# Optimization experiments

Hardware: AMD Instinct MI355X
Metric: run time of the kernel (lower is better)

Reference implementation:

```python
import jax, jax.numpy as jnp
import numpy as np

N = 400000        # pixel nodes (B images ~224x224)
E = 3200000       # edges, avg degree 8
B = 8             # images
NUM_SP = 150      # superpixels per image (<= 196, per assert)
S = B * NUM_SP    # total superpixel segments
GRID = 14 * 14    # fixed 14x14 grid = 196 slots
DIMS = [24, 8, 16, 32, 64, 64]  # conv_out_dim=24 -> channels//8 ... channels=64


def setup_inputs():
    key = jax.random.key(0)
    ks = jax.random.split(key, 16)
    inp = {}
    inp["x"] = jax.random.normal(ks[0], (N, DIMS[0]), jnp.float32)
    inp["edge_index"] = jax.random.randint(ks[1], (2, E), 0, N, jnp.int32)
    inp["batch_idx"] = jnp.sort(jax.random.randint(ks[2], (N,), 0, S, jnp.int32))
    inp["num_sp"] = jnp.full((B,), NUM_SP, jnp.int32)
    for i in range(5):
        fi, fo = DIMS[i], DIMS[i + 1]
        inp[f"W{i+1}"] = jax.random.normal(ks[3 + i], (fi, fo), jnp.float32) * (2.0 / fi) ** 0.5
        inp[f"b{i+1}"] = jnp.zeros((fo,), jnp.float32)
        inp[f"g{i+1}"] = jnp.ones((fo,), jnp.float32)
        inp[f"be{i+1}"] = jnp.zeros((fo,), jnp.float32)
    C = DIMS[-1]
    inp["Wp"] = jax.random.normal(ks[9], (4 * C, C), jnp.float32) * (2.0 / (4 * C)) ** 0.5
    inp["bp"] = jnp.zeros((C,), jnp.float32)
    return inp


def _forward(x, edge_index, batch_idx, num_sp, layers, Wp, bp):
    n = x.shape[0]
    # GCNConv: add self-loops, symmetric normalization D^-1/2 (A+I) D^-1/2
    loop = jnp.arange(n, dtype=edge_index.dtype)
    src = jnp.concatenate([edge_index[0], loop])
    dst = jnp.concatenate([edge_index[1], loop])
    deg = jax.ops.segment_sum(jnp.ones_like(dst, dtype=jnp.float32), dst, num_segments=n)
    dis = jax.lax.rsqrt(deg)  # deg >= 1 due to self-loops
    norm = dis[src] * dis[dst]  # [E+N]

    h = x
    for i, (W, b, g, be) in enumerate(layers):
        h = h @ W                                                   # [N, fo]
        h = jax.ops.segment_sum(h[src] * norm[:, None], dst, num_segments=n) + b
        # BatchNorm (training mode: batch stats over all nodes)
        mu = h.mean(axis=0)
        var = h.var(axis=0)
        h = g * (h - mu) * jax.lax.rsqrt(var + 1e-5) + be
        if i < 4:  # last BN feeds the aggregator directly (no ReLU)
            h = jax.nn.relu(h)

    # MultiAggregation(['mean','min','max','std'], mode='proj') over superpixel ids
    cnt = jnp.maximum(jax.ops.segment_sum(jnp.ones((n, 1), jnp.float32), batch_idx, num_segments=S), 1.0)
    sm = jax.ops.segment_sum(h, batch_idx, num_segments=S)
    sm2 = jax.ops.segment_sum(h * h, batch_idx, num_segments=S)
    mean = sm / cnt
    std = jnp.sqrt(jax.nn.relu(sm2 / cnt - mean * mean) + 1e-5)  # PyG StdAggregation
    mn = jax.ops.segment_min(h, batch_idx, num_segments=S)
    mx = jax.ops.segment_max(h, batch_idx, num_segments=S)
    agg = jnp.concatenate([mean, mn, mx, std], axis=1) @ Wp + bp  # [S, C]

    # padding_reshape_layer: pack per-image superpixel rows into [B, C, 14, 14]
    offs = jnp.cumsum(num_sp) - num_sp                # start row of each image
    pos = jnp.arange(GRID, dtype=num_sp.dtype)
    idx = jnp.clip(offs[:, None] + pos[None, :], 0, S - 1)  # [B, 196]
    mask = pos[None, :] < num_sp[:, None]
    feats = jnp.where(mask[..., None], agg[idx], 0.0)       # [B, 196, C]
    C = agg.shape[1]
    # torch: reshape(14,14,C) then transpose(0,2) -> y[c,j,i] = x[i,j,c]
    return feats.reshape(B, 14, 14, C).transpose(0, 3, 2, 1)


def reference(x, edge_index, batch_idx, num_sp,
              W1, b1, g1, be1, W2, b2, g2, be2, W3, b3, g3, be3,
              W4, b4, g4, be4, W5, b5, g5, be5, Wp, bp):
    layers = [(W1, b1, g1, be1), (W2, b2, g2, be2), (W3, b3, g3, be3),
              (W4, b4, g4, be4), (W5, b5, g5, be5)]
    return _forward(x, edge_index, batch_idx, num_sp, layers, Wp, bp)
```

## Files before the change

kernel.cpp:

```cpp
#include <hip/hip_runtime.h>
#include <hip/hip_fp16.h>

#define TPB 256
#define BSH 9
#define BUCK (1 << BSH)
#define NBMAX 1024
#define CAP 6144

using f16x8 = __attribute__((ext_vector_type(8))) _Float16;
using f32x4 = __attribute__((ext_vector_type(4))) float;


union H8 { uint4 u; __half2 h[4]; };
union H4 { uint2 u; __half2 h[2]; };

__device__ inline void h8_to_f(const H8 v, float4& a, float4& b) {
    float2 f0 = __half22float2(v.h[0]);
    float2 f1 = __half22float2(v.h[1]);
    float2 f2 = __half22float2(v.h[2]);
    float2 f3 = __half22float2(v.h[3]);
    a = make_float4(f0.x, f0.y, f1.x, f1.y);
    b = make_float4(f2.x, f2.y, f3.x, f3.y);
}
__device__ inline H8 f_to_h8(float4 a, float4 b) {
    H8 r;
    r.h[0] = __floats2half2_rn(a.x, a.y);
    r.h[1] = __floats2half2_rn(a.z, a.w);
    r.h[2] = __floats2half2_rn(b.x, b.y);
    r.h[3] = __floats2half2_rn(b.z, b.w);
    return r;
}
__device__ inline float4 f4z() { return make_float4(0.f, 0.f, 0.f, 0.f); }
__device__ inline float4 f4axpy(float4 a, float s, float4 c) {
    return make_float4(fmaf(a.x, s, c.x), fmaf(a.y, s, c.y), fmaf(a.z, s, c.z), fmaf(a.w, s, c.w));
}
__device__ inline float4 f4relu_aff(float4 h, float4 sc, float4 sb) {
    return make_float4(fmaxf(fmaf(h.x, sc.x, sb.x), 0.f), fmaxf(fmaf(h.y, sc.y, sb.y), 0.f),
                       fmaxf(fmaf(h.z, sc.z, sb.z), 0.f), fmaxf(fmaf(h.w, sc.w, sb.w), 0.f));
}


__global__ __launch_bounds__(256) void k_bcount(const int* __restrict__ dst, int E,
                                                int* __restrict__ bcount, int nb) {
    __shared__ int hist[NBMAX];
    for (int i = threadIdx.x; i < nb; i += 256) hist[i] = 0;
    __syncthreads();
    const int e0 = blockIdx.x * 8192;
#pragma unroll 4
    for (int k = 0; k < 32; ++k) {
        int e = e0 + k * 256 + threadIdx.x;
        if (e < E) atomicAdd(&hist[dst[e] >> BSH], 1);
    }
    __syncthreads();
    for (int i = threadIdx.x; i < nb; i += 256) {
        int h = hist[i];
        if (h) atomicAdd(&bcount[i], h);
    }
}

__global__ void k_bscan(const int* __restrict__ bcount, int* __restrict__ bbase,
                        int* __restrict__ bcur, int nb, int E, int* __restrict__ row_ptr,
                        int n) {
    if (threadIdx.x == 0 && blockIdx.x == 0) {
        int run = 0;
        for (int i = 0; i < nb; ++i) {
            bbase[i] = run;
            bcur[i] = run;
            run += bcount[i];
        }
        bbase[nb] = E;
        row_ptr[n] = E;
    }
}

__global__ __launch_bounds__(256) void k_partA(const int* __restrict__ src,
                                               const int* __restrict__ dst, int E,
                                               int* __restrict__ bcur, int* __restrict__ bin,
                                               int nb) {
    __shared__ int hist[NBMAX];
    __shared__ int base[NBMAX];
    for (int i = threadIdx.x; i < nb; i += 256) hist[i] = 0;
    __syncthreads();
    const int e0 = blockIdx.x * 8192;
#pragma unroll 4
    for (int k = 0; k < 32; ++k) {
        int e = e0 + k * 256 + threadIdx.x;
        if (e < E) atomicAdd(&hist[dst[e] >> BSH], 1);
    }
    __syncthreads();
    for (int i = threadIdx.x; i < nb; i += 256) {
        int h = hist[i];
        base[i] = h ? atomicAdd(&bcur[i], h) : 0;
        hist[i] = 0;
    }
    __syncthreads();
#pragma unroll 4
    for (int k = 0; k < 32; ++k) {
        int e = e0 + k * 256 + threadIdx.x;
        if (e < E) {
            int d = dst[e];
            int b = d >> BSH;
            int off = atomicAdd(&hist[b], 1);
            bin[base[b] + off] = ((d & (BUCK - 1)) << 19) | src[e];
        }
    }
}

__global__ __launch_bounds__(256) void k_csr_bucket(const int* __restrict__ bin,
                                                    const int* __restrict__ bbase,
                                                    int* __restrict__ row_ptr,
                                                    float* __restrict__ dis,
                                                    int* __restrict__ csr_src, int n) {
    __shared__ int ldeg[BUCK];
    __shared__ int lcur[BUCK];
    __shared__ int ts[256];
    __shared__ int stage[CAP];
    const int b = blockIdx.x;
    const int node0 = b << BSH;
    const int nodes = min(BUCK, n - node0);
    const int ebeg = bbase[b], eend = bbase[b + 1];
    const int cnt = eend - ebeg;

    for (int i = threadIdx.x; i < BUCK; i += 256) ldeg[i] = 0;
    __syncthreads();
    for (int e = ebeg + threadIdx.x; e < eend; e += 256)
        atomicAdd(&ldeg[bin[e] >> 19], 1);
    __syncthreads();

    const int b2 = threadIdx.x * 2;
    int v0 = ldeg[b2], v1 = ldeg[b2 + 1];
    ts[threadIdx.x] = v0 + v1;
    __syncthreads();
    for (int off = 1; off < 256; off <<= 1) {
        int t = (threadIdx.x >= off) ? ts[threadIdx.x - off] : 0;
        __syncthreads();
        ts[threadIdx.x] += t;
        __syncthreads();
    }
    int o0 = (threadIdx.x == 0) ? 0 : ts[threadIdx.x - 1];
    int o1 = o0 + v0;
    lcur[b2] = o0;
    lcur[b2 + 1] = o1;
    if (b2 < nodes) {
        row_ptr[node0 + b2] = ebeg + o0;
        dis[node0 + b2] = rsqrtf((float)(v0 + 1));
    }
    if (b2 + 1 < nodes) {
        row_ptr[node0 + b2 + 1] = ebeg + o1;
        dis[node0 + b2 + 1] = rsqrtf((float)(v1 + 1));
    }
    __syncthreads();

    for (int e = ebeg + threadIdx.x; e < eend; e += 256) {
        int p = bin[e];
        int pos = atomicAdd(&lcur[p >> 19], 1);
        int s = p & 0x7FFFF;
        if (pos < CAP) stage[pos] = s;
        else csr_src[ebeg + pos] = s;
    }
    __syncthreads();
    int m = cnt < CAP ? cnt : CAP;
    for (int i = threadIdx.x; i < m; i += 256) csr_src[ebeg + i] = stage[i];
}


template <int FI, int FO, bool STATS, bool IN_F32>
__global__ __launch_bounds__(TPB) void k_mm_v(const void* __restrict__ tin,
                                              const float* __restrict__ W,
                                              __half* __restrict__ z,
                                              float* __restrict__ stats, int n) {
    constexpr int GROUPS = FO / 8;
    constexpr int NPB = (TPB / GROUPS) * 4;
    __shared__ float sW[FI * FO];
    __shared__ float sred[STATS ? TPB * 16 : 1];
    for (int i = threadIdx.x; i < FI * FO; i += TPB) sW[i] = W[i];
    __syncthreads();

    const int g = threadIdx.x % GROUPS;
    const int nl = threadIdx.x / GROUPS;
    const int nbase = blockIdx.x * NPB + nl * 4;

    float4 acc0[4], acc1[4];
#pragma unroll
    for (int j = 0; j < 4; ++j) { acc0[j] = f4z(); acc1[j] = f4z(); }

    for (int k = 0; k < FI; k += 4) {
        float4 wv0[4], wv1[4];
#pragma unroll
        for (int kk = 0; kk < 4; ++kk) {
            wv0[kk] = *(const float4*)&sW[(k + kk) * FO + g * 8];
            wv1[kk] = *(const float4*)&sW[(k + kk) * FO + g * 8 + 4];
        }
#pragma unroll
        for (int j = 0; j < 4; ++j) {
            int node = nbase + j;
            float rk[4] = {0.f, 0.f, 0.f, 0.f};
            if (node < n) {
                if (IN_F32) {
                    float4 rv = *(const float4*)((const float*)tin + (size_t)node * FI + k);
                    rk[0] = rv.x; rk[1] = rv.y; rk[2] = rv.z; rk[3] = rv.w;
                } else {
                    H4 hv;
                    hv.u = *(const uint2*)((const __half*)tin + (size_t)node * FI + k);
                    float2 f0 = __half22float2(hv.h[0]);
                    float2 f1 = __half22float2(hv.h[1]);
                    rk[0] = f0.x; rk[1] = f0.y; rk[2] = f1.x; rk[3] = f1.y;
                }
            }
#pragma unroll
            for (int kk = 0; kk < 4; ++kk) {
                acc0[j] = f4axpy(wv0[kk], rk[kk], acc0[j]);
                acc1[j] = f4axpy(wv1[kk], rk[kk], acc1[j]);
            }
        }
    }

#pragma unroll
    for (int j = 0; j < 4; ++j) {
        int node = nbase + j;
        if (node < n) {
            H8 o = f_to_h8(acc0[j], acc1[j]);
            *(uint4*)(z + (size_t)node * FO + g * 8) = o.u;
        }
    }

    if (STATS) {
        float4 s0 = f4z(), s1 = f4z(), q0 = f4z(), q1 = f4z();
#pragma unroll
        for (int j = 0; j < 4; ++j) {
            s0.x += acc0[j].x; s0.y += acc0[j].y; s0.z += acc0[j].z; s0.w += acc0[j].w;
            s1.x += acc1[j].x; s1.y += acc1[j].y; s1.z += acc1[j].z; s1.w += acc1[j].w;
            q0.x = fmaf(acc0[j].x, acc0[j].x, q0.x); q0.y = fmaf(acc0[j].y, acc0[j].y, q0.y);
            q0.z = fmaf(acc0[j].z, acc0[j].z, q0.z); q0.w = fmaf(acc0[j].w, acc0[j].w, q0.w);
            q1.x = fmaf(acc1[j].x, acc1[j].x, q1.x); q1.y = fmaf(acc1[j].y, acc1[j].y, q1.y);
            q1.z = fmaf(acc1[j].z, acc1[j].z, q1.z); q1.w = fmaf(acc1[j].w, acc1[j].w, q1.w);
        }
        float* slot = &sred[threadIdx.x * 16];
        *(float4*)(slot + 0) = s0;
        *(float4*)(slot + 4) = s1;
        *(float4*)(slot + 8) = q0;
        *(float4*)(slot + 12) = q1;
        __syncthreads();
        if (threadIdx.x < FO * 2) {
            int c = threadIdx.x % FO;
            int m = threadIdx.x / FO;
            int g2 = c / 8, ci = c % 8;
            float a = 0.f;
            for (int nl2 = 0; nl2 < TPB / GROUPS; ++nl2)
                a += sred[(nl2 * GROUPS + g2) * 16 + m * 8 + ci];
            atomicAdd(&stats[m * FO + c], a);
        }
    }
}


template <int FI>
__global__ __launch_bounds__(256) void k_mm_mfma(const __half* __restrict__ tin,
                                                 const float* __restrict__ W,
                                                 __half* __restrict__ z,
                                                 float* __restrict__ stats, int n) {
    constexpr int KC = FI / 32;
    constexpr int RSW = FI + 8;
    __shared__ _Float16 wt[64 * RSW];
    __shared__ float sstat[2][4][64];
    for (int i = threadIdx.x; i < FI * 64; i += 256) {
        int k = i >> 6, nn = i & 63;
        wt[nn * RSW + k] = (_Float16)W[i];
    }
    __syncthreads();

    const int lane = threadIdx.x & 63;
    const int wv = threadIdx.x >> 6;
    const int quad = lane >> 4;
    const int mcol = lane & 15;
    const int rowbase = blockIdx.x * 256 + wv * 64;

    f16x8 b[4][KC];
#pragma unroll
    for (int t = 0; t < 4; ++t)
#pragma unroll
        for (int c = 0; c < KC; ++c)
            b[t][c] = *(const f16x8*)&wt[(t * 16 + mcol) * RSW + c * 32 + quad * 8];

    float s[4] = {0.f, 0.f, 0.f, 0.f}, q[4] = {0.f, 0.f, 0.f, 0.f};

#pragma unroll
    for (int rt = 0; rt < 4; ++rt) {
        const int row0 = rowbase + rt * 16;
        const int arow = row0 + mcol;
        f16x8 a[KC];
#pragma unroll
        for (int c = 0; c < KC; ++c) {
            if (arow < n)
                a[c] = *(const f16x8*)((const _Float16*)tin + (size_t)arow * FI + c * 32 +
                                       quad * 8);
            else
                a[c] = f16x8{0, 0, 0, 0, 0, 0, 0, 0};
        }
        f32x4 acc[4];
#pragma unroll
        for (int t = 0; t < 4; ++t) acc[t] = f32x4{0.f, 0.f, 0.f, 0.f};
#pragma unroll
        for (int t = 0; t < 4; ++t)
#pragma unroll
            for (int c = 0; c < KC; ++c)
                acc[t] = __builtin_amdgcn_mfma_f32_16x16x32_f16(a[c], b[t][c], acc[t], 0, 0, 0);

#pragma unroll
        for (int t = 0; t < 4; ++t)
#pragma unroll
            for (int r = 0; r < 4; ++r) {
                int row = row0 + quad * 4 + r;
                if (row < n) z[(size_t)row * 64 + t * 16 + mcol] = __float2half(acc[t][r]);
            }
#pragma unroll
        for (int t = 0; t < 4; ++t) {
            s[t] += acc[t][0] + acc[t][1] + acc[t][2] + acc[t][3];
            q[t] += acc[t][0] * acc[t][0] + acc[t][1] * acc[t][1] + acc[t][2] * acc[t][2] +
                    acc[t][3] * acc[t][3];
        }
    }

#pragma unroll
    for (int off = 16; off < 64; off <<= 1) {
#pragma unroll
        for (int t = 0; t < 4; ++t) {
            s[t] += __shfl_xor(s[t], off, 64);
            q[t] += __shfl_xor(q[t], off, 64);
        }
    }
    if (lane < 16) {
#pragma unroll
        for (int t = 0; t < 4; ++t) {
            sstat[0][wv][t * 16 + lane] = s[t];
            sstat[1][wv][t * 16 + lane] = q[t];
        }
    }
    __syncthreads();
    if (threadIdx.x < 128) {
        int c = threadIdx.x & 63, m = threadIdx.x >> 6;
        float a4 = sstat[m][0][c] + sstat[m][1][c] + sstat[m][2][c] + sstat[m][3][c];
        atomicAdd(&stats[m * 64 + c], a4);
    }
}


template <int F, bool AFFINE, bool STATS>
__global__ __launch_bounds__(TPB) void k_gather(const int* __restrict__ row_ptr,
                                                const int* __restrict__ csr_src,
                                                const float* __restrict__ dis,
                                                const __half* __restrict__ z,
                                                __half* __restrict__ t,
                                                const float* __restrict__ stats_in,
                                                const float* __restrict__ gg,
                                                const float* __restrict__ be, float inv_n,
                                                float* __restrict__ stats_out, int n) {
    constexpr int GW = (F < 16) ? F : 16;
    constexpr int PARTS = F / GW;
    constexpr int NV = GW / 4;
    constexpr int NL = GW / 8;
    __shared__ float sred[STATS ? TPB * 16 : 1];
    int tid = blockIdx.x * blockDim.x + threadIdx.x;
    int node = tid / PARTS;
    int part = tid % PARTS;
    bool active = node < n;
    if (!STATS && !active) return;
    const int cbase = part * GW;

    float4 sc[NV], sb[NV];
    if (AFFINE) {
#pragma unroll
        for (int v = 0; v < NV; ++v) {
            float scv[4], sbv[4];
#pragma unroll
            for (int u = 0; u < 4; ++u) {
                int c = cbase + v * 4 + u;
                float mu = stats_in[c] * inv_n;
                float var = stats_in[F + c] * inv_n - mu * mu;
                float s = gg[c] * rsqrtf(var + 1e-5f);
                scv[u] = s;
                sbv[u] = fmaf(-mu, s, be[c]);
            }
            sc[v] = make_float4(scv[0], scv[1], scv[2], scv[3]);
            sb[v] = make_float4(sbv[0], sbv[1], sbv[2], sbv[3]);
        }
    }

    float4 acc[NV];
#pragma unroll
    for (int v = 0; v < NV; ++v) acc[v] = f4z();

    if (active) {
        float dn = dis[node];
        float w0 = dn * dn;
        {
            const uint4* zp = (const uint4*)(z + (size_t)node * F + cbase);
#pragma unroll
            for (int l = 0; l < NL; ++l) {
                H8 hv; hv.u = zp[l];
                float4 a, b;
                h8_to_f(hv, a, b);
                if (AFFINE) { a = f4relu_aff(a, sc[2 * l], sb[2 * l]); b = f4relu_aff(b, sc[2 * l + 1], sb[2 * l + 1]); }
                acc[2 * l] = f4axpy(a, w0, acc[2 * l]);
                acc[2 * l + 1] = f4axpy(b, w0, acc[2 * l + 1]);
            }
        }
        int beg = row_ptr[node], end = row_ptr[node + 1];
        int j = beg;
        for (; j + 1 < end; j += 2) {
            int s0 = csr_src[j], s1 = csr_src[j + 1];
            float wA = dn * dis[s0];
            float wB = dn * dis[s1];
            const uint4* pA = (const uint4*)(z + (size_t)s0 * F + cbase);
            const uint4* pB = (const uint4*)(z + (size_t)s1 * F + cbase);
            uint4 rA[NL], rB[NL];
#pragma unroll
            for (int l = 0; l < NL; ++l) { rA[l] = pA[l]; rB[l] = pB[l]; }
#pragma unroll
            for (int l = 0; l < NL; ++l) {
                H8 hv; float4 a, b;
                hv.u = rA[l];
                h8_to_f(hv, a, b);
                if (AFFINE) { a = f4relu_aff(a, sc[2 * l], sb[2 * l]); b = f4relu_aff(b, sc[2 * l + 1], sb[2 * l + 1]); }
                acc[2 * l] = f4axpy(a, wA, acc[2 * l]);
                acc[2 * l + 1] = f4axpy(b, wA, acc[2 * l + 1]);
                hv.u = rB[l];
                h8_to_f(hv, a, b);
                if (AFFINE) { a = f4relu_aff(a, sc[2 * l], sb[2 * l]); b = f4relu_aff(b, sc[2 * l + 1], sb[2 * l + 1]); }
                acc[2 * l] = f4axpy(a, wB, acc[2 * l]);
                acc[2 * l + 1] = f4axpy(b, wB, acc[2 * l + 1]);
            }
        }
        if (j < end) {
            int s0 = csr_src[j];
            float wA = dn * dis[s0];
            const uint4* pA = (const uint4*)(z + (size_t)s0 * F + cbase);
#pragma unroll
            for (int l = 0; l < NL; ++l) {
                H8 hv; hv.u = pA[l];
                float4 a, b;
                h8_to_f(hv, a, b);
                if (AFFINE) { a = f4relu_aff(a, sc[2 * l], sb[2 * l]); b = f4relu_aff(b, sc[2 * l + 1], sb[2 * l + 1]); }
                acc[2 * l] = f4axpy(a, wA, acc[2 * l]);
                acc[2 * l + 1] = f4axpy(b, wA, acc[2 * l + 1]);
            }
        }
        uint4* tp = (uint4*)(t + (size_t)node * F + cbase);
#pragma unroll
        for (int l = 0; l < NL; ++l) tp[l] = f_to_h8(acc[2 * l], acc[2 * l + 1]).u;
    }

    if (STATS) {
        float* slot = &sred[threadIdx.x * 16];
        *(float4*)(slot + 0) = acc[0];
        *(float4*)(slot + 4) = acc[1];
        float4 q0 = make_float4(acc[0].x * acc[0].x, acc[0].y * acc[0].y, acc[0].z * acc[0].z,
                                acc[0].w * acc[0].w);
        float4 q1 = make_float4(acc[1].x * acc[1].x, acc[1].y * acc[1].y, acc[1].z * acc[1].z,
                                acc[1].w * acc[1].w);
        *(float4*)(slot + 8) = q0;
        *(float4*)(slot + 12) = q1;
        __syncthreads();
        if (threadIdx.x < 16) {
            int c = threadIdx.x % 8;
            int m = threadIdx.x / 8;
            float a = 0.f;
            for (int t2 = 0; t2 < TPB; ++t2) a += sred[t2 * 16 + m * 8 + c];
            atomicAdd(&stats_out[m * 8 + c], a);
        }
    }
}


__device__ inline int bsearch_seg(const int* __restrict__ bidx, int n, int s) {
    int lo = 0, hi = n;
    while (lo < hi) {
        int mid = (lo + hi) >> 1;
        if (bidx[mid] < s) lo = mid + 1; else hi = mid;
    }
    return lo;
}

__global__ __launch_bounds__(TPB) void k_seg_reduce(const __half* __restrict__ z,
                                                    const int* __restrict__ bidx, int n,
                                                    float* __restrict__ aggin,
                                                    const float* __restrict__ stats,
                                                    const float* __restrict__ gg,
                                                    const float* __restrict__ be, float inv_n) {
    __shared__ int sbounds[2];
    int s = blockIdx.x;
    if (threadIdx.x < 2) sbounds[threadIdx.x] = bsearch_seg(bidx, n, s + threadIdx.x);
    __syncthreads();
    int start = sbounds[0], end = sbounds[1];
    int c = threadIdx.x & 63;
    float mu = stats[c] * inv_n;
    float var = stats[64 + c] * inv_n - mu * mu;
    float scv = gg[c] * rsqrtf(var + 1e-5f);
    float sbv = fmaf(-mu, scv, be[c]);
    int r0 = start + (threadIdx.x >> 6);
    float sm = 0.f, sm2 = 0.f, mn = INFINITY, mx = -INFINITY;
    for (int r = r0; r < end; r += 4) {
        float v = fmaf(__half2float(z[(size_t)r * 64 + c]), scv, sbv);
        sm += v;
        sm2 = fmaf(v, v, sm2);
        mn = fminf(mn, v);
        mx = fmaxf(mx, v);
    }
    __shared__ float s_sm[TPB], s_sm2[TPB], s_mn[TPB], s_mx[TPB];
    s_sm[threadIdx.x] = sm;
    s_sm2[threadIdx.x] = sm2;
    s_mn[threadIdx.x] = mn;
    s_mx[threadIdx.x] = mx;
    __syncthreads();
    if (threadIdx.x < 64) {
        for (int t = threadIdx.x + 64; t < TPB; t += 64) {
            sm += s_sm[t];
            sm2 += s_sm2[t];
            mn = fminf(mn, s_mn[t]);
            mx = fmaxf(mx, s_mx[t]);
        }
        int count = end - start;
        float cnt = (float)(count > 0 ? count : 1);
        float mean = sm / cnt;
        float var2 = sm2 / cnt - mean * mean;
        if (var2 < 0.f) var2 = 0.f;
        float sd = sqrtf(var2 + 1e-5f);
        if (count <= 0) { mn = 0.f; mx = 0.f; }
        aggin[s * 256 + c] = mean;
        aggin[s * 256 + 64 + c] = mn;
        aggin[s * 256 + 128 + c] = mx;
        aggin[s * 256 + 192 + c] = sd;
    }
}

__global__ __launch_bounds__(64) void k_proj(const float* __restrict__ aggin,
                                             const float* __restrict__ Wp,
                                             const float* __restrict__ bp,
                                             float* __restrict__ proj) {
    __shared__ float sA[256];
    int s = blockIdx.x;
    int j = threadIdx.x;
    for (int k = j; k < 256; k += 64) sA[k] = aggin[s * 256 + k];
    __syncthreads();
    float acc = bp[j];
#pragma unroll 8
    for (int k = 0; k < 256; ++k) acc = fmaf(sA[k], Wp[k * 64 + j], acc);
    proj[s * 64 + j] = acc;
}

__global__ void k_pack(const float* __restrict__ proj, const int* __restrict__ num_sp,
                       float* __restrict__ out, int B, int S) {
    int idx = blockIdx.x * blockDim.x + threadIdx.x;
    int total = B * 64 * 196;
    if (idx >= total) return;
    int ii = idx % 14;
    int jj = (idx / 14) % 14;
    int c = (idx / 196) % 64;
    int b = idx / (196 * 64);
    int p = ii * 14 + jj;
    int off = 0;
    for (int k = 0; k < b; ++k) off += num_sp[k];
    float v = 0.f;
    if (p < num_sp[b]) {
        int s = off + p;
        if (s > S - 1) s = S - 1;
        v = proj[s * 64 + c];
    }
    out[idx] = v;
}


extern "C" void kernel_launch(void* const* d_in, const int* in_sizes, int n_in,
                              void* d_out, int out_size, void* d_ws, size_t ws_size,
                              hipStream_t stream) {
    const float* x = (const float*)d_in[0];
    const int* ei = (const int*)d_in[1];
    const int* bidx = (const int*)d_in[2];
    const int* num_sp = (const int*)d_in[3];
    const float* Wl[5], * Gl[5], * BEl[5];
    for (int i = 0; i < 5; ++i) {
        Wl[i] = (const float*)d_in[4 + 4 * i];
        Gl[i] = (const float*)d_in[6 + 4 * i];
        BEl[i] = (const float*)d_in[7 + 4 * i];
    }
    const float* Wp = (const float*)d_in[24];
    const float* bp = (const float*)d_in[25];

    const int n = in_sizes[0] / 24;
    const int E = in_sizes[1] / 2;
    const int B = in_sizes[3];
    const int S = 1200;
    const int* src = ei;
    const int* dst = ei + E;
    const float inv_n = 1.0f / (float)n;
    const int nb = (n + BUCK - 1) >> BSH;

    char* w = (char*)d_ws;
    __half* bufZ = (__half*)w;  w += (size_t)n * 64 * 2;
    __half* bufT = (__half*)w;  w += (size_t)n * 64 * 2;
    float* dis = (float*)w;     w += (size_t)n * 4;
    int* row_ptr = (int*)w;     w += (size_t)(n + 64) * 4;
    int* csr_src = (int*)w;     w += (size_t)E * 4;
    int* bin = (int*)w;         w += (size_t)E * 4;
    int* bcount = (int*)w;      w += (size_t)(nb + 64) * 4;
    int* bbase = (int*)w;       w += (size_t)(nb + 64) * 4;
    int* bcur = (int*)w;        w += (size_t)(nb + 64) * 4;
    float* stats_all = (float*)w; w += 5 * 128 * 4;
    float* aggin = (float*)w;   w += (size_t)S * 256 * 4;
    float* proj = (float*)w;    w += (size_t)S * 64 * 4;
    float* st0 = stats_all;
    float* st1 = stats_all + 128;
    float* st2 = stats_all + 256;
    float* st3 = stats_all + 384;
    float* st4 = stats_all + 512;

    hipMemsetAsync(bcount, 0, (size_t)nb * 4, stream);
    hipMemsetAsync(stats_all, 0, 5 * 128 * 4, stream);
    k_bcount<<<(E + 8191) / 8192, 256, 0, stream>>>(dst, E, bcount, nb);
    k_bscan<<<1, 64, 0, stream>>>(bcount, bbase, bcur, nb, E, row_ptr, n);
    k_partA<<<(E + 8191) / 8192, 256, 0, stream>>>(src, dst, E, bcur, bin, nb);
    k_csr_bucket<<<nb, 256, 0, stream>>>(bin, bbase, row_ptr, dis, csr_src, n);

    k_mm_v<24, 8, false, true><<<(n + 1023) / 1024, TPB, 0, stream>>>(x, Wl[0], bufT, nullptr, n);
    k_gather<8, false, true><<<(n + TPB - 1) / TPB, TPB, 0, stream>>>(
        row_ptr, csr_src, dis, bufT, bufZ, nullptr, nullptr, nullptr, inv_n, st0, n);

    k_gather<8, true, false><<<(n + TPB - 1) / TPB, TPB, 0, stream>>>(
        row_ptr, csr_src, dis, bufZ, bufT, st0, Gl[0], BEl[0], inv_n, nullptr, n);
    k_mm_v<8, 16, true, false><<<(n + 511) / 512, TPB, 0, stream>>>(bufT, Wl[1], bufZ, st1, n);

    k_gather<16, true, false><<<(n + TPB - 1) / TPB, TPB, 0, stream>>>(
        row_ptr, csr_src, dis, bufZ, bufT, st1, Gl[1], BEl[1], inv_n, nullptr, n);
    k_mm_v<16, 32, true, false><<<(n + 255) / 256, TPB, 0, stream>>>(bufT, Wl[2], bufZ, st2, n);

    k_gather<32, true, false><<<(2 * n + TPB - 1) / TPB, TPB, 0, stream>>>(
        row_ptr, csr_src, dis, bufZ, bufT, st2, Gl[2], BEl[2], inv_n, nullptr, n);
    k_mm_mfma<32><<<(n + 255) / 256, 256, 0, stream>>>(bufT, Wl[3], bufZ, st3, n);

    k_gather<64, true, false><<<(4 * n + TPB - 1) / TPB, TPB, 0, stream>>>(
        row_ptr, csr_src, dis, bufZ, bufT, st3, Gl[3], BEl[3], inv_n, nullptr, n);
    k_mm_mfma<64><<<(n + 255) / 256, 256, 0, stream>>>(bufT, Wl[4], bufZ, st4, n);

    k_seg_reduce<<<S, TPB, 0, stream>>>(bufZ, bidx, n, aggin, st4, Gl[4], BEl[4], inv_n);
    k_proj<<<S, 64, 0, stream>>>(aggin, Wp, bp, proj);
    int total_out = B * 64 * 196;
    k_pack<<<(total_out + TPB - 1) / TPB, TPB, 0, stream>>>(proj, num_sp, (float*)d_out, B, S);
}
```

Measured before the change: 942.8 us.

## Fuse gather aggregation with MFMA matmul for the last two GCN layers

New measurement: 906.6 us. 3.8% less time.

```diff
diff --git a/kernel.cpp b/kernel.cpp
--- a/kernel.cpp
+++ b/kernel.cpp
@@ -254,18 +254,116 @@
 }
 
 
-template <int FI>
-__global__ __launch_bounds__(256) void k_mm_mfma(const __half* __restrict__ tin,
-                                                 const float* __restrict__ W,
-                                                 __half* __restrict__ z,
-                                                 float* __restrict__ stats, int n) {
+template <int FI, int ROWS>
+__global__ __launch_bounds__(256) void k_gmm(const int* __restrict__ row_ptr,
+                                             const int* __restrict__ csr_src,
+                                             const float* __restrict__ dis,
+                                             const __half* __restrict__ zin,
+                                             const float* __restrict__ W,
+                                             const float* __restrict__ stats_in,
+                                             const float* __restrict__ gg,
+                                             const float* __restrict__ be, float inv_n,
+                                             __half* __restrict__ zout,
+                                             float* __restrict__ stats_out, int n) {
+    constexpr int RSW = FI + 8;
+    constexpr int RST = FI + 8;
+    constexpr int PARTS = FI / 16;
     constexpr int KC = FI / 32;
-    constexpr int RSW = FI + 8;
+    constexpr int RT = ROWS / 64;
+    constexpr int NTASK = ROWS * PARTS / 256;
     __shared__ _Float16 wt[64 * RSW];
+    __shared__ _Float16 ttile[ROWS * RST];
+    __shared__ float saff[2 * FI];
     __shared__ float sstat[2][4][64];
+
     for (int i = threadIdx.x; i < FI * 64; i += 256) {
         int k = i >> 6, nn = i & 63;
         wt[nn * RSW + k] = (_Float16)W[i];
+    }
+    if (threadIdx.x < FI) {
+        int c = threadIdx.x;
+        float mu = stats_in[c] * inv_n;
+        float var = stats_in[FI + c] * inv_n - mu * mu;
+        float s = gg[c] * rsqrtf(var + 1e-5f);
+        saff[c] = s;
+        saff[FI + c] = fmaf(-mu, s, be[c]);
+    }
+    __syncthreads();
+
+    const int nbase = blockIdx.x * ROWS;
+
+#pragma unroll
+    for (int it = 0; it < NTASK; ++it) {
+        int tt = it * 256 + threadIdx.x;
+        int nl = tt / PARTS;
+        int part = tt % PARTS;
+        int node = nbase + nl;
+        int cbase = part * 16;
+        float4 sc[4], sb[4];
+#pragma unroll
+        for (int v = 0; v < 4; ++v) {
+            sc[v] = *(const float4*)&saff[cbase + v * 4];
+            sb[v] = *(const float4*)&saff[FI + cbase + v * 4];
+        }
+        float4 acc[4] = {f4z(), f4z(), f4z(), f4z()};
+        if (node < n) {
+            float dn = dis[node];
+            float w0 = dn * dn;
+            {
+                const uint4* zp = (const uint4*)(zin + (size_t)node * FI + cbase);
+#pragma unroll
+                for (int l = 0; l < 2; ++l) {
+                    H8 hv; hv.u = zp[l];
+                    float4 a, b;
+                    h8_to_f(hv, a, b);
+                    a = f4relu_aff(a, sc[2 * l], sb[2 * l]);
+                    b = f4relu_aff(b, sc[2 * l + 1], sb[2 * l + 1]);
+                    acc[2 * l] = f4axpy(a, w0, acc[2 * l]);
+                    acc[2 * l + 1] = f4axpy(b, w0, acc[2 * l + 1]);
+                }
+            }
+            int beg = row_ptr[node], end = row_ptr[node + 1];
+            int j = beg;
+            for (; j + 1 < end; j += 2) {
+                int s0 = csr_src[j], s1 = csr_src[j + 1];
+                float wA = dn * dis[s0];
+                float wB = dn * dis[s1];
+                const uint4* pA = (const uint4*)(zin + (size_t)s0 * FI + cbase);
+                const uint4* pB = (const uint4*)(zin + (size_t)s1 * FI + cbase);
+                uint4 rA0 = pA[0], rA1 = pA[1], rB0 = pB[0], rB1 = pB[1];
+                H8 hv; float4 a, b;
+                hv.u = rA0; h8_to_f(hv, a, b);
+                a = f4relu_aff(a, sc[0], sb[0]); b = f4relu_aff(b, sc[1], sb[1]);
+                acc[0] = f4axpy(a, wA, acc[0]); acc[1] = f4axpy(b, wA, acc[1]);
+                hv.u = rA1; h8_to_f(hv, a, b);
+                a = f4relu_aff(a, sc[2], sb[2]); b = f4relu_aff(b, sc[3], sb[3]);
+                acc[2] = f4axpy(a, wA, acc[2]); acc[3] = f4axpy(b, wA, acc[3]);
+                hv.u = rB0; h8_to_f(hv, a, b);
+                a = f4relu_aff(a, sc[0], sb[0]); b = f4relu_aff(b, sc[1], sb[1]);
+                acc[0] = f4axpy(a, wB, acc[0]); acc[1] = f4axpy(b, wB, acc[1]);
+                hv.u = rB1; h8_to_f(hv, a, b);
+                a = f4relu_aff(a, sc[2], sb[2]); b = f4relu_aff(b, sc[3], sb[3]);
+                acc[2] = f4axpy(a, wB, acc[2]); acc[3] = f4axpy(b, wB, acc[3]);
+            }
+            if (j < end) {
+                int s0 = csr_src[j];
+                float wA = dn * dis[s0];
+                const uint4* pA = (const uint4*)(zin + (size_t)s0 * FI + cbase);
+#pragma unroll
+                for (int l = 0; l < 2; ++l) {
+                    H8 hv; hv.u = pA[l];
+                    float4 a, b;
+                    h8_to_f(hv, a, b);
+                    a = f4relu_aff(a, sc[2 * l], sb[2 * l]);
+                    b = f4relu_aff(b, sc[2 * l + 1], sb[2 * l + 1]);
+                    acc[2 * l] = f4axpy(a, wA, acc[2 * l]);
+                    acc[2 * l + 1] = f4axpy(b, wA, acc[2 * l + 1]);
+                }
+            }
+        }
+        _Float16* tp = &ttile[nl * RST + cbase];
+        *(uint4*)(tp) = f_to_h8(acc[0], acc[1]).u;
+        *(uint4*)(tp + 8) = f_to_h8(acc[2], acc[3]).u;
     }
     __syncthreads();
 
@@ -273,30 +371,23 @@
     const int wv = threadIdx.x >> 6;
     const int quad = lane >> 4;
     const int mcol = lane & 15;
-    const int rowbase = blockIdx.x * 256 + wv * 64;
-
-    f16x8 b[4][KC];
+
+    f16x8 bf[4][KC];
 #pragma unroll
     for (int t = 0; t < 4; ++t)
 #pragma unroll
         for (int c = 0; c < KC; ++c)
-            b[t][c] = *(const f16x8*)&wt[(t * 16 + mcol) * RSW + c * 32 + quad * 8];
+            bf[t][c] = *(const f16x8*)&wt[(t * 16 + mcol) * RSW + c * 32 + quad * 8];
 
     float s[4] = {0.f, 0.f, 0.f, 0.f}, q[4] = {0.f, 0.f, 0.f, 0.f};
 
 #pragma unroll
-    for (int rt = 0; rt < 4; ++rt) {
-        const int row0 = rowbase + rt * 16;
-        const int arow = row0 + mcol;
+    for (int rt = 0; rt < RT; ++rt) {
+        const int lrow0 = wv * RT * 16 + rt * 16;
         f16x8 a[KC];
 #pragma unroll
-        for (int c = 0; c < KC; ++c) {
-            if (arow < n)
-                a[c] = *(const f16x8*)((const _Float16*)tin + (size_t)arow * FI + c * 32 +
-                                       quad * 8);
-            else
-                a[c] = f16x8{0, 0, 0, 0, 0, 0, 0, 0};
-        }
+        for (int c = 0; c < KC; ++c)
+            a[c] = *(const f16x8*)&ttile[(lrow0 + mcol) * RST + c * 32 + quad * 8];
         f32x4 acc[4];
 #pragma unroll
         for (int t = 0; t < 4; ++t) acc[t] = f32x4{0.f, 0.f, 0.f, 0.f};
@@ -304,14 +395,14 @@
         for (int t = 0; t < 4; ++t)
 #pragma unroll
             for (int c = 0; c < KC; ++c)
-                acc[t] = __builtin_amdgcn_mfma_f32_16x16x32_f16(a[c], b[t][c], acc[t], 0, 0, 0);
+                acc[t] = __builtin_amdgcn_mfma_f32_16x16x32_f16(a[c], bf[t][c], acc[t], 0, 0, 0);
 
 #pragma unroll
         for (int t = 0; t < 4; ++t)
 #pragma unroll
             for (int r = 0; r < 4; ++r) {
-                int row = row0 + quad * 4 + r;
-                if (row < n) z[(size_t)row * 64 + t * 16 + mcol] = __float2half(acc[t][r]);
+                int row = nbase + lrow0 + quad * 4 + r;
+                if (row < n) zout[(size_t)row * 64 + t * 16 + mcol] = __float2half(acc[t][r]);
             }
 #pragma unroll
         for (int t = 0; t < 4; ++t) {
@@ -340,7 +431,7 @@
     if (threadIdx.x < 128) {
         int c = threadIdx.x & 63, m = threadIdx.x >> 6;
         float a4 = sstat[m][0][c] + sstat[m][1][c] + sstat[m][2][c] + sstat[m][3][c];
-        atomicAdd(&stats[m * 64 + c], a4);
+        atomicAdd(&stats_out[m * 64 + c], a4);
     }
 }
 
@@ -407,31 +498,37 @@
         }
         int beg = row_ptr[node], end = row_ptr[node + 1];
         int j = beg;
-        for (; j + 1 < end; j += 2) {
-            int s0 = csr_src[j], s1 = csr_src[j + 1];
+        for (; j + 3 < end; j += 4) {
+            int s0 = csr_src[j], s1 = csr_src[j + 1], s2 = csr_src[j + 2], s3 = csr_src[j + 3];
             float wA = dn * dis[s0];
             float wB = dn * dis[s1];
+            float wC = dn * dis[s2];
+            float wD = dn * dis[s3];
             const uint4* pA = (const uint4*)(z + (size_t)s0 * F + cbase);
             const uint4* pB = (const uint4*)(z + (size_t)s1 * F + cbase);
-            uint4 rA[NL], rB[NL];
-#pragma unroll
-            for (int l = 0; l < NL; ++l) { rA[l] = pA[l]; rB[l] = pB[l]; }
+            const uint4* pC = (const uint4*)(z + (size_t)s2 * F + cbase);
+            const uint4* pD = (const uint4*)(z + (size_t)s3 * F + cbase);
+            uint4 rA[NL], rB[NL], rC[NL], rD[NL];
+#pragma unroll
+            for (int l = 0; l < NL; ++l) { rA[l] = pA[l]; rB[l] = pB[l]; rC[l] = pC[l]; rD[l] = pD[l]; }
 #pragma unroll
             for (int l = 0; l < NL; ++l) {
                 H8 hv; float4 a, b;
-                hv.u = rA[l];
-                h8_to_f(hv, a, b);
+                hv.u = rA[l]; h8_to_f(hv, a, b);
                 if (AFFINE) { a = f4relu_aff(a, sc[2 * l], sb[2 * l]); b = f4relu_aff(b, sc[2 * l + 1], sb[2 * l + 1]); }
-                acc[2 * l] = f4axpy(a, wA, acc[2 * l]);
-                acc[2 * l + 1] = f4axpy(b, wA, acc[2 * l + 1]);
-                hv.u = rB[l];
-                h8_to_f(hv, a, b);
+                acc[2 * l] = f4axpy(a, wA, acc[2 * l]); acc[2 * l + 1] = f4axpy(b, wA, acc[2 * l + 1]);
+                hv.u = rB[l]; h8_to_f(hv, a, b);
                 if (AFFINE) { a = f4relu_aff(a, sc[2 * l], sb[2 * l]); b = f4relu_aff(b, sc[2 * l + 1], sb[2 * l + 1]); }
-                acc[2 * l] = f4axpy(a, wB, acc[2 * l]);
-                acc[2 * l + 1] = f4axpy(b, wB, acc[2 * l + 1]);
-            }
-        }
-        if (j < end) {
+                acc[2 * l] = f4axpy(a, wB, acc[2 * l]); acc[2 * l + 1] = f4axpy(b, wB, acc[2 * l + 1]);
+                hv.u = rC[l]; h8_to_f(hv, a, b);
+                if (AFFINE) { a = f4relu_aff(a, sc[2 * l], sb[2 * l]); b = f4relu_aff(b, sc[2 * l + 1], sb[2 * l + 1]); }
+                acc[2 * l] = f4axpy(a, wC, acc[2 * l]); acc[2 * l + 1] = f4axpy(b, wC, acc[2 * l + 1]);
+                hv.u = rD[l]; h8_to_f(hv, a, b);
+                if (AFFINE) { a = f4relu_aff(a, sc[2 * l], sb[2 * l]); b = f4relu_aff(b, sc[2 * l + 1], sb[2 * l + 1]); }
+                acc[2 * l] = f4axpy(a, wD, acc[2 * l]); acc[2 * l + 1] = f4axpy(b, wD, acc[2 * l + 1]);
+            }
+        }
+        for (; j < end; ++j) {
             int s0 = csr_src[j];
             float wA = dn * dis[s0];
             const uint4* pA = (const uint4*)(z + (size_t)s0 * F + cbase);
@@ -633,13 +730,10 @@
         row_ptr, csr_src, dis, bufZ, bufT, st1, Gl[1], BEl[1], inv_n, nullptr, n);
     k_mm_v<16, 32, true, false><<<(n + 255) / 256, TPB, 0, stream>>>(bufT, Wl[2], bufZ, st2, n);
 
-    k_gather<32, true, false><<<(2 * n + TPB - 1) / TPB, TPB, 0, stream>>>(
-        row_ptr, csr_src, dis, bufZ, bufT, st2, Gl[2], BEl[2], inv_n, nullptr, n);
-    k_mm_mfma<32><<<(n + 255) / 256, 256, 0, stream>>>(bufT, Wl[3], bufZ, st3, n);
-
-    k_gather<64, true, false><<<(4 * n + TPB - 1) / TPB, TPB, 0, stream>>>(
-        row_ptr, csr_src, dis, bufZ, bufT, st3, Gl[3], BEl[3], inv_n, nullptr, n);
-    k_mm_mfma<64><<<(n + 255) / 256, 256, 0, stream>>>(bufT, Wl[4], bufZ, st4, n);
+    k_gmm<32, 256><<<(n + 255) / 256, 256, 0, stream>>>(
+        row_ptr, csr_src, dis, bufZ, Wl[3], st2, Gl[2], BEl[2], inv_n, bufT, st3, n);
+    k_gmm<64, 192><<<(n + 191) / 192, 256, 0, stream>>>(
+        row_ptr, csr_src, dis, bufT, Wl[4], st3, Gl[3], BEl[3], inv_n, bufZ, st4, n);
 
     k_seg_reduce<<<S, TPB, 0, stream>>>(bufZ, bidx, n, aggin, st4, Gl[4], BEl[4], inv_n);
     k_proj<<<S, 64, 0, stream>>>(aggin, Wp, bp, proj);
```
